# Kernel tuning notes

Measured on AMD Instinct MI355X. Metric: run time of the kernel, lower is better.

The kernel has to match this reference:

```python
import jax, jax.numpy as jnp
import numpy as np

# dims
F, V, E, NIN, NOUT = 4, 4, 64, 1024, 1024
M = NIN + 2
# args constants
GMIN, GMAX, EPS, PGMIN = 0.01, 1.0, 0.1, 0.1
ETA2 = 0.25          # ACT[0].eta_fault[0,2]
ACT_T, NEG_T = 1.0, 1.0

# stand-in printed-electronics nonlinearities (ACT list and INV list)
_ACT = [lambda z: jax.nn.sigmoid(4.0 * (z - 0.5)), lambda z: jnp.tanh(z)]
_INV = [lambda a: 1.0 - a, lambda a: jax.nn.sigmoid(4.0 * (0.5 - a))]


def setup_inputs() -> dict:
    key = jax.random.key(0)
    ks = jax.random.split(key, 8)
    a = jax.random.uniform(ks[0], (F, V, E, NIN), jnp.float32)
    theta = jax.random.uniform(ks[1], (M, NOUT), jnp.float32) / 100.0 + GMIN
    theta = theta.at[-1, :].add(GMAX)
    theta = theta.at[-2, :].set(ETA2 / (1.0 - ETA2) * (theta[:-2, :].sum(0) + theta[-1, :]))
    coeff_act = jax.random.uniform(ks[2], (2, NOUT), jnp.float32, minval=-0.5, maxval=0.5)
    coeff_neg = jax.random.uniform(ks[3], (2, M), jnp.float32, minval=-0.5, maxval=0.5)
    noise_u = jax.random.uniform(ks[4], (F, V, M, NOUT), jnp.float32)
    gum = lambda k, s: -jnp.log(-jnp.log(jax.random.uniform(k, s, jnp.float32) + 1e-20) + 1e-20)
    gum_act = gum(ks[5], (2, NOUT))
    gum_neg = gum(ks[6], (2, M))
    fault_mask = jnp.ones((F, M, NOUT), jnp.float32)
    return dict(a=a, theta_=theta, coeff_act=coeff_act, coeff_neg=coeff_neg,
                noise_u=noise_u, gum_act=gum_act, gum_neg=gum_neg, fault_mask=fault_mask)


def _st_clip(x, lo, hi):
    sg = jax.lax.stop_gradient
    return x + sg(jnp.clip(x, lo, hi) - x)


def _gumbel_st(c, g, temp):
    # clamp, gumbel-softmax, hard argmax with straight-through estimator
    sg = jax.lax.stop_gradient
    cc = _st_clip(c, -1.0, 1.0)
    alpha = jax.nn.softmax((cc + g) / temp, axis=0)
    hard = jax.nn.one_hot(jnp.argmax(alpha, 0), c.shape[0], axis=0, dtype=alpha.dtype)
    return sg(hard) + alpha - sg(alpha)


def _forward(a, theta_, coeff_act, coeff_neg, noise_u, gum_act, gum_neg, fault_mask):
    sg = jax.lax.stop_gradient
    # theta property: clamp, zero small magnitudes (straight-through)
    tc = _st_clip(theta_, -GMAX, GMAX)
    tz = jnp.where(jnp.abs(tc) < GMIN, 0.0, tc)
    theta = sg(tz) + tc - sg(tc)
    # theta_noisy [F,V,M,N]: repeat + multiplicative uniform noise + fault mask
    tn = theta[None, None] * ((noise_u * 2.0 - 1.0) * EPS + 1.0) * fault_mask[:, None]
    at = jnp.abs(tn)
    W = at / (at.sum(axis=2, keepdims=True) + 1e-10)
    pos = (tn >= 0).astype(W.dtype)
    neg = 1.0 - pos
    # a_extend [F,V,E,M]: append bias-one and zero columns
    ones = jnp.ones(a.shape[:3] + (1,), a.dtype)
    ax = jnp.concatenate([a, ones, jnp.zeros_like(ones)], axis=-1)
    beta = _gumbel_st(coeff_neg, gum_neg, NEG_T)      # [2,M]
    an = beta[0] * _INV[0](ax) + beta[1] * _INV[1](ax)
    an = an.at[..., -1].set(0.0)
    z = (jnp.einsum('fvem,fvmn->fven', ax, W * pos)
         + jnp.einsum('fvem,fvmn->fven', an, W * neg))
    # MAC_power: vectorized expansion of sum_{f,v,m,n} g[m,n]*||sel - y||^2 over e
    gi = jnp.abs(tc)
    gt = gi * (PGMIN / gi.min(axis=0, keepdims=True))  # g_tilde [M,N]
    p = sg(pos)
    q = 1.0 - p
    AA = jnp.einsum('fvem,fvem->fvm', ax, ax)
    BB = jnp.einsum('fvem,fvem->fvm', an, an)
    AY = jnp.einsum('fvem,fven->fvmn', ax, z)
    BY = jnp.einsum('fvem,fven->fvmn', an, z)
    YY = jnp.einsum('fven,fven->fvn', z, z)
    power = (jnp.einsum('mn,fvmn,fvm->', gt, p, AA)
             + jnp.einsum('mn,fvmn,fvm->', gt, q, BB)
             - 2.0 * (jnp.einsum('mn,fvmn,fvmn->', gt, p, AY)
                      + jnp.einsum('mn,fvmn,fvmn->', gt, q, BY))
             + jnp.einsum('n,fvn->', gt.sum(0), YY)) / (E * V * F)
    # Gumbel-mixed activation
    alpha = _gumbel_st(coeff_act, gum_act, ACT_T)      # [2,N]
    a_new = alpha[0] * _ACT[0](z) + alpha[1] * _ACT[1](z)
    return a_new, power


def reference(a, theta_, coeff_act, coeff_neg, noise_u, gum_act, gum_neg, fault_mask):
    return _forward(a, theta_, coeff_act, coeff_neg, noise_u, gum_act, gum_neg, fault_mask)
```

## Files before the change

kernel.cpp:

```cpp
#include <hip/hip_runtime.h>

typedef float f32x4 __attribute__((ext_vector_type(4)));
typedef short bf16x8 __attribute__((ext_vector_type(8)));

#define NE 64
#define ND 1024
#define MM 1026

#define WS_GMINP 1050624
#define WS_GSUMP 1083392
#define WS_AA    1642504
#define WS_BB    1658888
#define WS_TFG   1675272
#define WS_AXB   5877768
#define WS_ANB   6402056
#define POWER_IDX 1048576

__device__ __forceinline__ float frcp(float x) { return __builtin_amdgcn_rcpf(x); }
__device__ __forceinline__ unsigned f2b(float x) {
  unsigned u = __float_as_uint(x);
  u += 0x7FFF + ((u >> 16) & 1);
  return u >> 16;
}
__device__ __forceinline__ float b2f(unsigned b) { return __uint_as_float(b << 16); }
__device__ __forceinline__ float clamp1(float x) { return fminf(fmaxf(x, -1.f), 1.f); }

__global__ __launch_bounds__(256) void k_min(const float* __restrict__ theta_,
                                             float* __restrict__ ws,
                                             float* __restrict__ out) {
  int b = blockIdx.x, t = threadIdx.x;
  int n4 = t * 4;
  int m0 = b * 32, m1 = (b == 31) ? MM : m0 + 32;
  float mn0 = 1e30f, mn1 = 1e30f, mn2 = 1e30f, mn3 = 1e30f;
  for (int m = m0; m < m1; m++) {
    float4 tv = *(const float4*)(theta_ + m * ND + n4);
    mn0 = fminf(mn0, fabsf(clamp1(tv.x)));
    mn1 = fminf(mn1, fabsf(clamp1(tv.y)));
    mn2 = fminf(mn2, fabsf(clamp1(tv.z)));
    mn3 = fminf(mn3, fabsf(clamp1(tv.w)));
  }
  float4 mo = {mn0, mn1, mn2, mn3};
  *(float4*)(ws + WS_GMINP + b * ND + n4) = mo;
  if (b == 0 && t == 0) out[POWER_IDX] = 0.f;
}

__global__ __launch_bounds__(256) void k_pre(
    const float* __restrict__ a, const float* __restrict__ theta_,
    const float* __restrict__ fault, const float* __restrict__ coeff_neg,
    const float* __restrict__ gum_neg, float* __restrict__ ws) {
  int bid = blockIdx.x, t = threadIdx.x;
  __shared__ float la[256][8];
  __shared__ float lb[256][8];
  __shared__ float beta_l[32];

  if (bid < 512) {
    int kc = bid & 31, fv = bid >> 5;
    if (t < 32) {
      int m = kc * 32 + t;
      float c0 = clamp1(coeff_neg[m]);
      float c1 = clamp1(coeff_neg[MM + m]);
      beta_l[t] = ((c1 + gum_neg[MM + m]) > (c0 + gum_neg[m])) ? 1.f : 0.f;
    }
    __syncthreads();
    int em = t >> 6, l = t & 63;
    int e = em * 16 + (l & 15);
    int g = (l >> 4) & 3;
    int kk = kc * 32 + g * 4;
    const float* ap = a + ((size_t)fv * NE + e) * 1024;
    float4 x0 = *(const float4*)(ap + kk);
    float4 x1 = *(const float4*)(ap + kk + 16);
    float xs[8] = {x0.x, x0.y, x0.z, x0.w, x1.x, x1.y, x1.z, x1.w};
    unsigned axp[8], anp[8];
#pragma unroll
    for (int j = 0; j < 8; j++) {
      int mloc = g * 4 + ((j < 4) ? j : 12 + j);
      float x = xs[j];
      float bs = beta_l[mloc];
      float an = (bs != 0.f) ? frcp(1.f + __expf(fmaf(4.f, x, -2.f))) : (1.f - x);
      axp[j] = f2b(x);
      anp[j] = f2b(an);
      la[t][j] = x * x;
      lb[t][j] = an * an;
    }
    uint4 ox = {axp[0] | (axp[1] << 16), axp[2] | (axp[3] << 16),
                axp[4] | (axp[5] << 16), axp[6] | (axp[7] << 16)};
    uint4 on = {anp[0] | (anp[1] << 16), anp[2] | (anp[3] << 16),
                anp[4] | (anp[5] << 16), anp[6] | (anp[7] << 16)};
    size_t bidx = ((size_t)(fv * 32 + kc) * 4 + em) * 64 + l;
    ((uint4*)(ws + WS_AXB))[bidx] = ox;
    ((uint4*)(ws + WS_ANB))[bidx] = on;
    __syncthreads();
    if (t < 32) {
      int g2 = (t >> 2) & 3, j2 = (t & 3) + 4 * (t >> 4);
      float sa = 0.f, sb = 0.f;
#pragma unroll
      for (int em2 = 0; em2 < 4; em2++)
#pragma unroll
        for (int i = 0; i < 16; i++) {
          sa += la[em2 * 64 + g2 * 16 + i][j2];
          sb += lb[em2 * 64 + g2 * 16 + i][j2];
        }
      ws[WS_AA + fv * 1024 + kc * 32 + t] = sa;
      ws[WS_BB + fv * 1024 + kc * 32 + t] = sb;
    }
  } else {
    int r = bid - 512;
    int f = r >> 5, chunk = r & 31;
    int n4 = t * 4;
    float g0 = 1e30f, g1 = 1e30f, g2 = 1e30f, g3 = 1e30f;
#pragma unroll 8
    for (int c = 0; c < 32; c++) {
      float4 v = *(const float4*)(ws + WS_GMINP + c * ND + n4);
      g0 = fminf(g0, v.x); g1 = fminf(g1, v.y);
      g2 = fminf(g2, v.z); g3 = fminf(g3, v.w);
    }
    float s0 = 0.1f * frcp(g0), s1 = 0.1f * frcp(g1);
    float s2 = 0.1f * frcp(g2), s3 = 0.1f * frcp(g3);
    int m0 = chunk * 32, m1 = (chunk == 31) ? MM : m0 + 32;
    unsigned* tfg = (unsigned*)(ws + WS_TFG) + (size_t)f * MM * ND;
    const float* fslab = fault + (size_t)f * MM * ND;
    float a0 = 0.f, a1 = 0.f, a2 = 0.f, a3 = 0.f;
    for (int m = m0; m < m1; m++) {
      float4 tv = *(const float4*)(theta_ + m * ND + n4);
      float4 fl = *(const float4*)(fslab + (size_t)m * ND + n4);
      float c0 = clamp1(tv.x), c1 = clamp1(tv.y), c2 = clamp1(tv.z), c3 = clamp1(tv.w);
      float z0 = fabsf(c0), z1 = fabsf(c1), z2 = fabsf(c2), z3 = fabsf(c3);
      float q0 = z0 * s0, q1 = z1 * s1, q2 = z2 * s2, q3 = z3 * s3;
      float w0 = (z0 < 0.01f ? 0.f : c0) * fl.x;
      float w1 = (z1 < 0.01f ? 0.f : c1) * fl.y;
      float w2 = (z2 < 0.01f ? 0.f : c2) * fl.z;
      float w3 = (z3 < 0.01f ? 0.f : c3) * fl.w;
      uint4 o;
      o.x = (f2b(q0) << 16) | f2b(w0);
      o.y = (f2b(q1) << 16) | f2b(w1);
      o.z = (f2b(q2) << 16) | f2b(w2);
      o.w = (f2b(q3) << 16) | f2b(w3);
      *(uint4*)(tfg + (size_t)m * ND + n4) = o;
      a0 += q0; a1 += q1; a2 += q2; a3 += q3;
    }
    if (f == 0) {
      float4 so = {a0, a1, a2, a3};
      *(float4*)(ws + WS_GSUMP + chunk * ND + n4) = so;
    }
  }
}

union U8 { uint4 u; bf16x8 h; };

#define SLOAD(S, MC)                                                       \
  {                                                                        \
    _Pragma("unroll") for (int r = 0; r < 8; r++) {                        \
      size_t row = (size_t)((MC) + mb + r) * ND;                           \
      uA##S[r] = nslab[row + n0 + nin];                                    \
      uB##S[r] = nslab[row + n0 + 16 + nin];                               \
      tgA##S[r] = tslab[row + n0 + nin];                                   \
      tgB##S[r] = tslab[row + n0 + 16 + nin];                              \
    }                                                                      \
  }

#define AABBLOAD(MC)                                                       \
  {                                                                        \
    aa0 = *(const float4*)(AAp + (MC) + mb);                               \
    aa1 = *(const float4*)(AAp + (MC) + mb + 4);                           \
    bb0 = *(const float4*)(BBp + (MC) + mb);                               \
    bb1 = *(const float4*)(BBp + (MC) + mb + 4);                           \
  }

#define SWRITE(P, S)                                                       \
  {                                                                        \
    float aas[8] = {aa0.x, aa0.y, aa0.z, aa0.w, aa1.x, aa1.y, aa1.z, aa1.w};\
    float bbs[8] = {bb0.x, bb0.y, bb0.z, bb0.w, bb1.x, bb1.y, bb1.z, bb1.w};\
    unsigned wpu[2][8], wnu[2][8], gpu[2][8], gqu[2][8];                   \
    _Pragma("unroll") for (int h = 0; h < 2; h++) {                        \
      _Pragma("unroll") for (int r = 0; r < 8; r++) {                      \
        unsigned tg = h ? tgB##S[r] : tgA##S[r];                           \
        float u = h ? uB##S[r] : uA##S[r];                                 \
        unsigned neg = (tg >> 15) & 1;                                     \
        float aw = b2f(tg & 0x7FFF) * fmaf(u, 0.2f, 0.9f);                 \
        if (h) sacc1 += aw; else sacc0 += aw;                              \
        unsigned wb = f2b(aw);                                             \
        unsigned gb = tg >> 16;                                            \
        wpu[h][r] = neg ? 0u : wb;  wnu[h][r] = neg ? wb : 0u;             \
        gpu[h][r] = neg ? 0u : gb;  gqu[h][r] = neg ? gb : 0u;             \
        float gtf = __uint_as_float(tg & 0xFFFF0000u);                     \
        pacc = fmaf(gtf, neg ? bbs[r] : aas[r], pacc);                     \
      }                                                                    \
    }                                                                      \
    _Pragma("unroll") for (int pn = 0; pn < 4; pn++) {                     \
      uint2* pp = (uint2*)&panels[P][pn][0];                               \
      _Pragma("unroll") for (int h = 0; h < 2; h++) {                      \
        const unsigned* v = pn == 0 ? wpu[h] : pn == 1 ? wnu[h]            \
                             : pn == 2 ? gpu[h] : gqu[h];                  \
        int s0i = ((c_s * 2 + h) * 64 + (g0 & 3) * 16 + nin) * 2 + j0q;    \
        int s1i = ((c_s * 2 + h) * 64 + ((g0 + 1) & 3) * 16 + nin) * 2 + j0q;\
        pp[s0i] = make_uint2(v[0] | (v[1] << 16), v[2] | (v[3] << 16));    \
        pp[s1i] = make_uint2(v[4] | (v[5] << 16), v[6] | (v[7] << 16));    \
      }                                                                    \
    }                                                                      \
  }

#define ALOAD(KS)                                                          \
  {                                                                        \
    _Pragma("unroll") for (int c = 0; c < 2; c++)                          \
      _Pragma("unroll") for (int mi = 0; mi < 4; mi++) {                   \
        size_t bi = ((size_t)(fv * 32 + (KS) * 2 + c) * 4 + mi) * 64 + l;  \
        axr[c][mi] = axbp[bi];                                             \
        anr[c][mi] = anbp[bi];                                             \
      }                                                                    \
  }

#define BMFMA(P)                                                           \
  {                                                                        \
    _Pragma("unroll") for (int c = 0; c < 2; c++) {                        \
      int bslot = (c * 2 + w) * 64 + l;                                    \
      U8 bwp, bwn, bgp, bgq;                                               \
      bwp.u = panels[P][0][bslot]; bwn.u = panels[P][1][bslot];            \
      bgp.u = panels[P][2][bslot]; bgq.u = panels[P][3][bslot];            \
      _Pragma("unroll") for (int mi = 0; mi < 4; mi++) {                   \
        U8 ax, an; ax.u = axr[c][mi]; an.u = anr[c][mi];                   \
        accz[mi] = __builtin_amdgcn_mfma_f32_16x16x32_bf16(ax.h, bwp.h, accz[mi], 0, 0, 0); \
        accz[mi] = __builtin_amdgcn_mfma_f32_16x16x32_bf16(an.h, bwn.h, accz[mi], 0, 0, 0); \
        accg[mi] = __builtin_amdgcn_mfma_f32_16x16x32_bf16(ax.h, bgp.h, accg[mi], 0, 0, 0); \
        accg[mi] = __builtin_amdgcn_mfma_f32_16x16x32_bf16(an.h, bgq.h, accg[mi], 0, 0, 0); \
      }                                                                    \
    }                                                                      \
  }

#define BAR() __syncthreads()

__global__ __launch_bounds__(128) void k_main(
    const float* __restrict__ noise, const float* __restrict__ ws_c,
    const float* __restrict__ coeff_act, const float* __restrict__ gum_act,
    const float* __restrict__ coeff_neg, const float* __restrict__ gum_neg,
    float* __restrict__ out) {
  const int tid = threadIdx.x;
  const int w = tid >> 6, l = tid & 63;
  const int fv = blockIdx.y, f = fv >> 2;
  const int n0 = blockIdx.x * 32;

  __shared__ uint4 panels[2][4][256];
  __shared__ float gsum_l[32];

  if (tid < 32) {
    float s = 0.f;
#pragma unroll 8
    for (int c = 0; c < 32; c++) s += ws_c[WS_GSUMP + c * ND + n0 + tid];
    gsum_l[tid] = s;
  }

  const int nin = tid & 15;
  const int mb = (tid >> 4) * 8;
  const int c_s = mb >> 5;
  const int g0 = (mb & 31) >> 2;
  const int j0q = (mb & 31) >> 4;
  const unsigned* tslab = (const unsigned*)(ws_c + WS_TFG) + (size_t)f * MM * ND;
  const float* nslab = noise + (size_t)fv * MM * ND;
  const float* AAp = ws_c + WS_AA + fv * 1024;
  const float* BBp = ws_c + WS_BB + fv * 1024;
  const uint4* axbp = (const uint4*)(ws_c + WS_AXB);
  const uint4* anbp = (const uint4*)(ws_c + WS_ANB);

  float pacc = 0.f, sacc0 = 0.f, sacc1 = 0.f;
  float uA0[8], uB0[8], uA1[8], uB1[8];
  unsigned tgA0[8], tgB0[8], tgA1[8], tgB1[8];
  float4 aa0, aa1, bb0, bb1;
  uint4 axr[2][4], anr[2][4];
  f32x4 accz[4] = {};
  f32x4 accg[4] = {};

  AABBLOAD(0);
  SLOAD(0, 0);
  SWRITE(0, 0);
  SLOAD(1, 64);
  BAR();

  for (int ks2 = 0; ks2 < 16; ks2 += 2) {
    ALOAD(ks2);
    AABBLOAD((ks2 + 1) * 64);
    if (ks2 < 14) SLOAD(0, (ks2 + 2) * 64);
    SWRITE(1, 1);
    BMFMA(0);
    BAR();
    ALOAD(ks2 + 1);
    if (ks2 < 14) {
      AABBLOAD((ks2 + 2) * 64);
      SLOAD(1, (ks2 + 3) * 64);
      SWRITE(0, 0);
    }
    BMFMA(1);
    BAR();
  }

  float* lds_f = (float*)&panels[0][0][0];
  lds_f[(tid >> 4) * 32 + nin] = sacc0;
  lds_f[(tid >> 4) * 32 + 16 + nin] = sacc1;
  __syncthreads();

  const int n_loc = w * 16 + (l & 15);
  const int n_e = n0 + n_loc;
  float S = 0.f;
#pragma unroll
  for (int mg = 0; mg < 8; mg++) S += lds_f[mg * 32 + n_loc];

  unsigned tg24 = tslab[(size_t)1024 * ND + n_e];
  unsigned tg25 = tslab[(size_t)1025 * ND + n_e];
  float u24 = nslab[(size_t)1024 * ND + n_e];
  float u25 = nslab[(size_t)1025 * ND + n_e];
  float w24 = b2f(tg24 & 0x7FFF) * fmaf(u24, 0.2f, 0.9f);
  float w25 = b2f(tg25 & 0x7FFF) * fmaf(u25, 0.2f, 0.9f);
  S += w24 + w25;
  const float invS = frcp(S + 1e-10f);

  float cn0 = clamp1(coeff_neg[1024]), cn1 = clamp1(coeff_neg[MM + 1024]);
  const float anb = ((cn1 + gum_neg[MM + 1024]) > (cn0 + gum_neg[1024]))
                        ? frcp(1.f + __expf(2.f)) : 0.f;
  float ca0 = clamp1(coeff_act[n_e]), ca1 = clamp1(coeff_act[ND + n_e]);
  const float alv = ((ca1 + gum_act[ND + n_e]) > (ca0 + gum_act[n_e])) ? 1.f : 0.f;

  unsigned neg24 = (tg24 >> 15) & 1;
  float sel24 = neg24 ? anb : 1.f;
  float ztail = w24 * invS * sel24;
  float gt24 = __uint_as_float(tg24 & 0xFFFF0000u);
  if (l < 16) pacc += 64.f * gt24 * sel24 * sel24;

  const float gsn = gsum_l[n_loc];
  float zsum = 0.f;
#pragma unroll
  for (int mi = 0; mi < 4; mi++) {
#pragma unroll
    for (int r = 0; r < 4; r++) {
      float z = accz[mi][r] * invS + ztail;
      zsum += z;
      pacc += gsn * z * z - 2.f * z * accg[mi][r];
      float s0v = frcp(1.f + __expf(fmaf(-4.f, z, 2.f)));
      float t1v = 1.f - 2.f * frcp(__expf(2.f * z) + 1.f);
      int e = mi * 16 + ((l >> 4) & 3) * 4 + r;
      out[((size_t)(fv * NE + e)) * ND + n_e] = (alv != 0.f) ? t1v : s0v;
    }
  }
  pacc -= 2.f * zsum * (gt24 * sel24);

  float* red = lds_f + 256;
  red[tid] = pacc;
  __syncthreads();
  for (int s = 64; s > 0; s >>= 1) {
    if (tid < s) red[tid] += red[tid + s];
    __syncthreads();
  }
  if (tid == 0) atomicAdd(out + POWER_IDX, red[0] * (1.f / 1024.f));
}

extern "C" void kernel_launch(void* const* d_in, const int* in_sizes, int n_in,
                              void* d_out, int out_size, void* d_ws, size_t ws_size,
                              hipStream_t stream) {
  const float* a = (const float*)d_in[0];
  const float* theta_ = (const float*)d_in[1];
  const float* coeff_act = (const float*)d_in[2];
  const float* coeff_neg = (const float*)d_in[3];
  const float* noise_u = (const float*)d_in[4];
  const float* gum_act = (const float*)d_in[5];
  const float* gum_neg = (const float*)d_in[6];
  const float* fault = (const float*)d_in[7];
  float* out = (float*)d_out;
  float* ws = (float*)d_ws;

  k_min<<<32, 256, 0, stream>>>(theta_, ws, out);
  k_pre<<<640, 256, 0, stream>>>(a, theta_, fault, coeff_neg, gum_neg, ws);
  k_main<<<dim3(32, 16), 128, 0, stream>>>(noise_u, ws, coeff_act, gum_act,
                                           coeff_neg, gum_neg, out);
}
```

Baseline: 195.5 us.

## Merge min kernel into pre-pass, defer g_tilde scaling, double main-kernel threads

Drops the separate k_min launch by storing unscaled |theta| in the packed theta/g buffer and computing per-column min and abs-sum partials inside k_pre. The PGMIN/min scale is applied later in k_main, so the theta-packing blocks no longer wait on the min reduction. The theta packing is also spread over more blocks with smaller row chunks. k_main goes from 128 to 256 threads: each thread streams half as many noise rows and each wave computes half the E rows, giving more waves per block to hide latency. The cost is extra partial-sum bookkeeping and a larger final reduction.

```diff
diff --git a/kernel.cpp b/kernel.cpp
--- a/kernel.cpp
+++ b/kernel.cpp
@@ -8,7 +8,7 @@
 #define MM 1026
 
 #define WS_GMINP 1050624
-#define WS_GSUMP 1083392
+#define WS_GABSP 1083392
 #define WS_AA    1642504
 #define WS_BB    1658888
 #define WS_TFG   1675272
@@ -25,36 +25,41 @@
 __device__ __forceinline__ float b2f(unsigned b) { return __uint_as_float(b << 16); }
 __device__ __forceinline__ float clamp1(float x) { return fminf(fmaxf(x, -1.f), 1.f); }
 
-__global__ __launch_bounds__(256) void k_min(const float* __restrict__ theta_,
-                                             float* __restrict__ ws,
-                                             float* __restrict__ out) {
-  int b = blockIdx.x, t = threadIdx.x;
-  int n4 = t * 4;
-  int m0 = b * 32, m1 = (b == 31) ? MM : m0 + 32;
-  float mn0 = 1e30f, mn1 = 1e30f, mn2 = 1e30f, mn3 = 1e30f;
-  for (int m = m0; m < m1; m++) {
-    float4 tv = *(const float4*)(theta_ + m * ND + n4);
-    mn0 = fminf(mn0, fabsf(clamp1(tv.x)));
-    mn1 = fminf(mn1, fabsf(clamp1(tv.y)));
-    mn2 = fminf(mn2, fabsf(clamp1(tv.z)));
-    mn3 = fminf(mn3, fabsf(clamp1(tv.w)));
-  }
-  float4 mo = {mn0, mn1, mn2, mn3};
-  *(float4*)(ws + WS_GMINP + b * ND + n4) = mo;
-  if (b == 0 && t == 0) out[POWER_IDX] = 0.f;
-}
-
 __global__ __launch_bounds__(256) void k_pre(
     const float* __restrict__ a, const float* __restrict__ theta_,
     const float* __restrict__ fault, const float* __restrict__ coeff_neg,
-    const float* __restrict__ gum_neg, float* __restrict__ ws) {
+    const float* __restrict__ gum_neg, float* __restrict__ ws,
+    float* __restrict__ out) {
   int bid = blockIdx.x, t = threadIdx.x;
   __shared__ float la[256][8];
   __shared__ float lb[256][8];
   __shared__ float beta_l[32];
 
   if (bid < 512) {
-    int kc = bid & 31, fv = bid >> 5;
+    int f = bid >> 7, chunk = bid & 127;
+    int m0 = chunk * 8, m1 = (chunk == 127) ? MM : m0 + 8;
+    unsigned* tfg = (unsigned*)(ws + WS_TFG) + (size_t)f * MM * ND;
+    const float* fslab = fault + (size_t)f * MM * ND;
+    int n4 = t * 4;
+    for (int m = m0; m < m1; m++) {
+      float4 tv = *(const float4*)(theta_ + m * ND + n4);
+      float4 fl = *(const float4*)(fslab + (size_t)m * ND + n4);
+      float c0 = clamp1(tv.x), c1 = clamp1(tv.y), c2 = clamp1(tv.z), c3 = clamp1(tv.w);
+      float z0 = fabsf(c0), z1 = fabsf(c1), z2 = fabsf(c2), z3 = fabsf(c3);
+      float w0 = (z0 < 0.01f ? 0.f : c0) * fl.x;
+      float w1 = (z1 < 0.01f ? 0.f : c1) * fl.y;
+      float w2 = (z2 < 0.01f ? 0.f : c2) * fl.z;
+      float w3 = (z3 < 0.01f ? 0.f : c3) * fl.w;
+      uint4 o;
+      o.x = (f2b(z0) << 16) | f2b(w0);
+      o.y = (f2b(z1) << 16) | f2b(w1);
+      o.z = (f2b(z2) << 16) | f2b(w2);
+      o.w = (f2b(z3) << 16) | f2b(w3);
+      *(uint4*)(tfg + (size_t)m * ND + n4) = o;
+    }
+  } else if (bid < 1024) {
+    int bb = bid - 512;
+    int kc = bb & 31, fv = bb >> 5;
     if (t < 32) {
       int m = kc * 32 + t;
       float c0 = clamp1(coeff_neg[m]);
@@ -104,44 +109,19 @@
       ws[WS_BB + fv * 1024 + kc * 32 + t] = sb;
     }
   } else {
-    int r = bid - 512;
-    int f = r >> 5, chunk = r & 31;
-    int n4 = t * 4;
-    float g0 = 1e30f, g1 = 1e30f, g2 = 1e30f, g3 = 1e30f;
-#pragma unroll 8
-    for (int c = 0; c < 32; c++) {
-      float4 v = *(const float4*)(ws + WS_GMINP + c * ND + n4);
-      g0 = fminf(g0, v.x); g1 = fminf(g1, v.y);
-      g2 = fminf(g2, v.z); g3 = fminf(g3, v.w);
-    }
-    float s0 = 0.1f * frcp(g0), s1 = 0.1f * frcp(g1);
-    float s2 = 0.1f * frcp(g2), s3 = 0.1f * frcp(g3);
+    int r = bid - 1024;
+    int ng = r & 3, chunk = r >> 2;
+    int n = ng * 256 + t;
     int m0 = chunk * 32, m1 = (chunk == 31) ? MM : m0 + 32;
-    unsigned* tfg = (unsigned*)(ws + WS_TFG) + (size_t)f * MM * ND;
-    const float* fslab = fault + (size_t)f * MM * ND;
-    float a0 = 0.f, a1 = 0.f, a2 = 0.f, a3 = 0.f;
+    float mn = 1e30f, sm = 0.f;
     for (int m = m0; m < m1; m++) {
-      float4 tv = *(const float4*)(theta_ + m * ND + n4);
-      float4 fl = *(const float4*)(fslab + (size_t)m * ND + n4);
-      float c0 = clamp1(tv.x), c1 = clamp1(tv.y), c2 = clamp1(tv.z), c3 = clamp1(tv.w);
-      float z0 = fabsf(c0), z1 = fabsf(c1), z2 = fabsf(c2), z3 = fabsf(c3);
-      float q0 = z0 * s0, q1 = z1 * s1, q2 = z2 * s2, q3 = z3 * s3;
-      float w0 = (z0 < 0.01f ? 0.f : c0) * fl.x;
-      float w1 = (z1 < 0.01f ? 0.f : c1) * fl.y;
-      float w2 = (z2 < 0.01f ? 0.f : c2) * fl.z;
-      float w3 = (z3 < 0.01f ? 0.f : c3) * fl.w;
-      uint4 o;
-      o.x = (f2b(q0) << 16) | f2b(w0);
-      o.y = (f2b(q1) << 16) | f2b(w1);
-      o.z = (f2b(q2) << 16) | f2b(w2);
-      o.w = (f2b(q3) << 16) | f2b(w3);
-      *(uint4*)(tfg + (size_t)m * ND + n4) = o;
-      a0 += q0; a1 += q1; a2 += q2; a3 += q3;
-    }
-    if (f == 0) {
-      float4 so = {a0, a1, a2, a3};
-      *(float4*)(ws + WS_GSUMP + chunk * ND + n4) = so;
-    }
+      float g = fabsf(clamp1(theta_[m * ND + n]));
+      mn = fminf(mn, g);
+      sm += g;
+    }
+    ws[WS_GMINP + chunk * ND + n] = mn;
+    ws[WS_GABSP + chunk * ND + n] = sm;
+    if (r == 0 && t == 0) out[POWER_IDX] = 0.f;
   }
 }
 
@@ -149,7 +129,7 @@
 
 #define SLOAD(S, MC)                                                       \
   {                                                                        \
-    _Pragma("unroll") for (int r = 0; r < 8; r++) {                        \
+    _Pragma("unroll") for (int r = 0; r < 4; r++) {                        \
       size_t row = (size_t)((MC) + mb + r) * ND;                           \
       uA##S[r] = nslab[row + n0 + nin];                                    \
       uB##S[r] = nslab[row + n0 + 16 + nin];                               \
@@ -161,18 +141,16 @@
 #define AABBLOAD(MC)                                                       \
   {                                                                        \
     aa0 = *(const float4*)(AAp + (MC) + mb);                               \
-    aa1 = *(const float4*)(AAp + (MC) + mb + 4);                           \
     bb0 = *(const float4*)(BBp + (MC) + mb);                               \
-    bb1 = *(const float4*)(BBp + (MC) + mb + 4);                           \
   }
 
 #define SWRITE(P, S)                                                       \
   {                                                                        \
-    float aas[8] = {aa0.x, aa0.y, aa0.z, aa0.w, aa1.x, aa1.y, aa1.z, aa1.w};\
-    float bbs[8] = {bb0.x, bb0.y, bb0.z, bb0.w, bb1.x, bb1.y, bb1.z, bb1.w};\
-    unsigned wpu[2][8], wnu[2][8], gpu[2][8], gqu[2][8];                   \
+    float aas[4] = {aa0.x, aa0.y, aa0.z, aa0.w};                           \
+    float bbs[4] = {bb0.x, bb0.y, bb0.z, bb0.w};                           \
+    unsigned wpu[2][4], wnu[2][4], gpu[2][4], gqu[2][4];                   \
     _Pragma("unroll") for (int h = 0; h < 2; h++) {                        \
-      _Pragma("unroll") for (int r = 0; r < 8; r++) {                      \
+      _Pragma("unroll") for (int r = 0; r < 4; r++) {                      \
         unsigned tg = h ? tgB##S[r] : tgA##S[r];                           \
         float u = h ? uB##S[r] : uA##S[r];                                 \
         unsigned neg = (tg >> 15) & 1;                                     \
@@ -182,8 +160,9 @@
         unsigned gb = tg >> 16;                                            \
         wpu[h][r] = neg ? 0u : wb;  wnu[h][r] = neg ? wb : 0u;             \
         gpu[h][r] = neg ? 0u : gb;  gqu[h][r] = neg ? gb : 0u;             \
-        float gtf = __uint_as_float(tg & 0xFFFF0000u);                     \
-        pacc = fmaf(gtf, neg ? bbs[r] : aas[r], pacc);                     \
+        float tca = b2f(gb);                                               \
+        float t1c = tca * (neg ? bbs[r] : aas[r]);                         \
+        if (h) pacc1b += t1c; else pacc1a += t1c;                          \
       }                                                                    \
     }                                                                      \
     _Pragma("unroll") for (int pn = 0; pn < 4; pn++) {                     \
@@ -192,9 +171,7 @@
         const unsigned* v = pn == 0 ? wpu[h] : pn == 1 ? wnu[h]            \
                              : pn == 2 ? gpu[h] : gqu[h];                  \
         int s0i = ((c_s * 2 + h) * 64 + (g0 & 3) * 16 + nin) * 2 + j0q;    \
-        int s1i = ((c_s * 2 + h) * 64 + ((g0 + 1) & 3) * 16 + nin) * 2 + j0q;\
         pp[s0i] = make_uint2(v[0] | (v[1] << 16), v[2] | (v[3] << 16));    \
-        pp[s1i] = make_uint2(v[4] | (v[5] << 16), v[6] | (v[7] << 16));    \
       }                                                                    \
     }                                                                      \
   }
@@ -202,8 +179,8 @@
 #define ALOAD(KS)                                                          \
   {                                                                        \
     _Pragma("unroll") for (int c = 0; c < 2; c++)                          \
-      _Pragma("unroll") for (int mi = 0; mi < 4; mi++) {                   \
-        size_t bi = ((size_t)(fv * 32 + (KS) * 2 + c) * 4 + mi) * 64 + l;  \
+      _Pragma("unroll") for (int mi = 0; mi < 2; mi++) {                   \
+        size_t bi = ((size_t)(fv * 32 + (KS) * 2 + c) * 4 + eh * 2 + mi) * 64 + l; \
         axr[c][mi] = axbp[bi];                                             \
         anr[c][mi] = anbp[bi];                                             \
       }                                                                    \
@@ -212,11 +189,11 @@
 #define BMFMA(P)                                                           \
   {                                                                        \
     _Pragma("unroll") for (int c = 0; c < 2; c++) {                        \
-      int bslot = (c * 2 + w) * 64 + l;                                    \
+      int bslot = (c * 2 + wn) * 64 + l;                                   \
       U8 bwp, bwn, bgp, bgq;                                               \
       bwp.u = panels[P][0][bslot]; bwn.u = panels[P][1][bslot];            \
       bgp.u = panels[P][2][bslot]; bgq.u = panels[P][3][bslot];            \
-      _Pragma("unroll") for (int mi = 0; mi < 4; mi++) {                   \
+      _Pragma("unroll") for (int mi = 0; mi < 2; mi++) {                   \
         U8 ax, an; ax.u = axr[c][mi]; an.u = anr[c][mi];                   \
         accz[mi] = __builtin_amdgcn_mfma_f32_16x16x32_bf16(ax.h, bwp.h, accz[mi], 0, 0, 0); \
         accz[mi] = __builtin_amdgcn_mfma_f32_16x16x32_bf16(an.h, bwn.h, accz[mi], 0, 0, 0); \
@@ -228,28 +205,42 @@
 
 #define BAR() __syncthreads()
 
-__global__ __launch_bounds__(128) void k_main(
+__global__ __launch_bounds__(256) void k_main(
     const float* __restrict__ noise, const float* __restrict__ ws_c,
     const float* __restrict__ coeff_act, const float* __restrict__ gum_act,
     const float* __restrict__ coeff_neg, const float* __restrict__ gum_neg,
     float* __restrict__ out) {
   const int tid = threadIdx.x;
-  const int w = tid >> 6, l = tid & 63;
+  const int w4 = tid >> 6, l = tid & 63;
+  const int wn = w4 & 1;
+  const int eh = w4 >> 1;
   const int fv = blockIdx.y, f = fv >> 2;
   const int n0 = blockIdx.x * 32;
 
   __shared__ uint4 panels[2][4][256];
-  __shared__ float gsum_l[32];
+  __shared__ float smin_l[32], gabs_l[32], s_l[32], gsum_l[32];
 
   if (tid < 32) {
+    float mn = 1e30f;
+#pragma unroll 8
+    for (int c = 0; c < 32; c++) mn = fminf(mn, ws_c[WS_GMINP + c * ND + n0 + tid]);
+    smin_l[tid] = mn;
+  } else if (tid < 64) {
+    int n = tid - 32;
     float s = 0.f;
 #pragma unroll 8
-    for (int c = 0; c < 32; c++) s += ws_c[WS_GSUMP + c * ND + n0 + tid];
-    gsum_l[tid] = s;
+    for (int c = 0; c < 32; c++) s += ws_c[WS_GABSP + c * ND + n0 + n];
+    gabs_l[n] = s;
+  }
+  __syncthreads();
+  if (tid < 32) {
+    float s = 0.1f * frcp(smin_l[tid]);
+    s_l[tid] = s;
+    gsum_l[tid] = s * gabs_l[tid];
   }
 
   const int nin = tid & 15;
-  const int mb = (tid >> 4) * 8;
+  const int mb = (tid >> 4) * 4;
   const int c_s = mb >> 5;
   const int g0 = (mb & 31) >> 2;
   const int j0q = (mb & 31) >> 4;
@@ -260,13 +251,13 @@
   const uint4* axbp = (const uint4*)(ws_c + WS_AXB);
   const uint4* anbp = (const uint4*)(ws_c + WS_ANB);
 
-  float pacc = 0.f, sacc0 = 0.f, sacc1 = 0.f;
-  float uA0[8], uB0[8], uA1[8], uB1[8];
-  unsigned tgA0[8], tgB0[8], tgA1[8], tgB1[8];
-  float4 aa0, aa1, bb0, bb1;
-  uint4 axr[2][4], anr[2][4];
-  f32x4 accz[4] = {};
-  f32x4 accg[4] = {};
+  float pacc = 0.f, pacc1a = 0.f, pacc1b = 0.f, sacc0 = 0.f, sacc1 = 0.f;
+  float uA0[4], uB0[4], uA1[4], uB1[4];
+  unsigned tgA0[4], tgB0[4], tgA1[4], tgB1[4];
+  float4 aa0, bb0;
+  uint4 axr[2][2], anr[2][2];
+  f32x4 accz[2] = {};
+  f32x4 accg[2] = {};
 
   AABBLOAD(0);
   SLOAD(0, 0);
@@ -296,12 +287,13 @@
   lds_f[(tid >> 4) * 32 + 16 + nin] = sacc1;
   __syncthreads();
 
-  const int n_loc = w * 16 + (l & 15);
+  const int n_loc = wn * 16 + (l & 15);
   const int n_e = n0 + n_loc;
   float S = 0.f;
 #pragma unroll
-  for (int mg = 0; mg < 8; mg++) S += lds_f[mg * 32 + n_loc];
-
+  for (int mg = 0; mg < 16; mg++) S += lds_f[mg * 32 + n_loc];
+
+  const float s_ne = s_l[n_loc];
   unsigned tg24 = tslab[(size_t)1024 * ND + n_e];
   unsigned tg25 = tslab[(size_t)1025 * ND + n_e];
   float u24 = nslab[(size_t)1024 * ND + n_e];
@@ -320,30 +312,31 @@
   unsigned neg24 = (tg24 >> 15) & 1;
   float sel24 = neg24 ? anb : 1.f;
   float ztail = w24 * invS * sel24;
-  float gt24 = __uint_as_float(tg24 & 0xFFFF0000u);
-  if (l < 16) pacc += 64.f * gt24 * sel24 * sel24;
+  float gt24 = b2f(tg24 >> 16) * s_ne;
+  if (l < 16 && eh == 0) pacc += 64.f * gt24 * sel24 * sel24;
 
   const float gsn = gsum_l[n_loc];
   float zsum = 0.f;
 #pragma unroll
-  for (int mi = 0; mi < 4; mi++) {
+  for (int mi = 0; mi < 2; mi++) {
 #pragma unroll
     for (int r = 0; r < 4; r++) {
       float z = accz[mi][r] * invS + ztail;
       zsum += z;
-      pacc += gsn * z * z - 2.f * z * accg[mi][r];
+      pacc += gsn * z * z - 2.f * z * (accg[mi][r] * s_ne);
       float s0v = frcp(1.f + __expf(fmaf(-4.f, z, 2.f)));
       float t1v = 1.f - 2.f * frcp(__expf(2.f * z) + 1.f);
-      int e = mi * 16 + ((l >> 4) & 3) * 4 + r;
+      int e = (eh * 2 + mi) * 16 + ((l >> 4) & 3) * 4 + r;
       out[((size_t)(fv * NE + e)) * ND + n_e] = (alv != 0.f) ? t1v : s0v;
     }
   }
   pacc -= 2.f * zsum * (gt24 * sel24);
-
-  float* red = lds_f + 256;
+  pacc += s_l[nin] * pacc1a + s_l[16 + nin] * pacc1b;
+
+  float* red = lds_f + 1024;
   red[tid] = pacc;
   __syncthreads();
-  for (int s = 64; s > 0; s >>= 1) {
+  for (int s = 128; s > 0; s >>= 1) {
     if (tid < s) red[tid] += red[tid + s];
     __syncthreads();
   }
@@ -364,8 +357,7 @@
   float* out = (float*)d_out;
   float* ws = (float*)d_ws;
 
-  k_min<<<32, 256, 0, stream>>>(theta_, ws, out);
-  k_pre<<<640, 256, 0, stream>>>(a, theta_, fault, coeff_neg, gum_neg, ws);
-  k_main<<<dim3(32, 16), 128, 0, stream>>>(noise_u, ws, coeff_act, gum_act,
+  k_pre<<<1152, 256, 0, stream>>>(a, theta_, fault, coeff_neg, gum_neg, ws, out);
+  k_main<<<dim3(32, 16), 256, 0, stream>>>(noise_u, ws, coeff_act, gum_act,
                                            coeff_neg, gum_neg, out);
 }
```

New measurement: 174.3 us. 10.8% less time.
